# Performance work log

Measured on AMD Instinct MI355X. Metric: run time of the kernel, lower is better.

Reference implementation:

```python
import jax, jax.numpy as jnp
from jax import lax
import numpy as np


def conv2d(x, w, b):
    # x: NCHW, w: OIHW, VALID padding, stride 1
    y = lax.conv_general_dilated(x, w, (1, 1), 'VALID',
                                 dimension_numbers=('NCHW', 'OIHW', 'NCHW'))
    return y + b[None, :, None, None]


def prelu(x, a):
    # per-channel PReLU, a: (C,)
    return jnp.where(x >= 0, x, a[None, :, None, None] * x)


def maxpool_ceil(x, k, s):
    # max pool with ceil_mode=True: pad right/bottom with -inf as needed
    H, W = x.shape[2], x.shape[3]
    def pad_amt(n):
        out = -(-(n - k) // s) + 1  # ceil
        return max(0, (out - 1) * s + k - n)
    ph, pw = pad_amt(H), pad_amt(W)
    return lax.reduce_window(x, -jnp.inf, lax.max,
                             (1, 1, k, k), (1, 1, s, s),
                             ((0, 0), (0, 0), (0, ph), (0, pw)))


def setup_inputs() -> dict:
    key = jax.random.key(0)
    ks = jax.random.split(key, 24)
    N = 2048
    x = jax.random.normal(ks[0], (N, 3, 48, 48), dtype=jnp.float32)

    def w_init(k, shape, fan_in):
        return jax.random.normal(k, shape, dtype=jnp.float32) * (1.0 / np.sqrt(fan_in))

    inp = {'x': x}
    inp['c1w'] = w_init(ks[1], (32, 3, 3, 3), 3 * 9)
    inp['c1b'] = jnp.zeros((32,), jnp.float32)
    inp['a1'] = jax.random.uniform(ks[2], (32,), jnp.float32, 0.1, 0.4)
    inp['c2w'] = w_init(ks[3], (64, 32, 3, 3), 32 * 9)
    inp['c2b'] = jnp.zeros((64,), jnp.float32)
    inp['a2'] = jax.random.uniform(ks[4], (64,), jnp.float32, 0.1, 0.4)
    inp['c3w'] = w_init(ks[5], (64, 64, 3, 3), 64 * 9)
    inp['c3b'] = jnp.zeros((64,), jnp.float32)
    inp['a3'] = jax.random.uniform(ks[6], (64,), jnp.float32, 0.1, 0.4)
    inp['c4w'] = w_init(ks[7], (128, 64, 2, 2), 64 * 4)
    inp['c4b'] = jnp.zeros((128,), jnp.float32)
    inp['a4'] = jax.random.uniform(ks[8], (128,), jnp.float32, 0.1, 0.4)
    inp['d5w'] = w_init(ks[9], (256, 1152), 1152)
    inp['d5b'] = jnp.zeros((256,), jnp.float32)
    inp['a5'] = jax.random.uniform(ks[10], (256,), jnp.float32, 0.1, 0.4)
    inp['d61w'] = w_init(ks[11], (2, 256), 256)
    inp['d61b'] = jnp.zeros((2,), jnp.float32)
    inp['d62w'] = w_init(ks[12], (4, 256), 256)
    inp['d62b'] = jnp.zeros((4,), jnp.float32)
    inp['d63w'] = w_init(ks[13], (10, 256), 256)
    inp['d63b'] = jnp.zeros((10,), jnp.float32)
    return inp


def reference(x, c1w, c1b, a1, c2w, c2b, a2, c3w, c3b, a3, c4w, c4b, a4,
              d5w, d5b, a5, d61w, d61b, d62w, d62b, d63w, d63b):
    h = prelu(conv2d(x, c1w, c1b), a1)          # [N,32,46,46]
    h = maxpool_ceil(h, 3, 2)                   # [N,32,23,23]
    h = prelu(conv2d(h, c2w, c2b), a2)          # [N,64,21,21]
    h = maxpool_ceil(h, 3, 2)                   # [N,64,10,10]
    h = prelu(conv2d(h, c3w, c3b), a3)          # [N,64,8,8]
    h = maxpool_ceil(h, 2, 2)                   # [N,64,4,4]
    h = prelu(conv2d(h, c4w, c4b), a4)          # [N,128,3,3]
    # torch: x.permute(0,3,2,1).contiguous().view(N,-1)
    h = jnp.transpose(h, (0, 3, 2, 1)).reshape(h.shape[0], -1)  # [N,1152]
    h = h @ d5w.T + d5b                         # [N,256]
    h = jnp.where(h >= 0, h, a5 * h)            # PReLU over features
    a = jax.nn.softmax(h @ d61w.T + d61b, axis=1)  # class probs [N,2]
    b = h @ d62w.T + d62b
    c = h @ d63w.T + d63b                       # landmarks [N,10]
    return (b, c, a)
```

## Files before the change

### kernel.cpp

```cpp
#include <hip/hip_runtime.h>
#include <hip/hip_bf16.h>
#include <hip/hip_fp16.h>
#include <stdint.h>

typedef short s16x8 __attribute__((ext_vector_type(8)));
typedef unsigned short u16x8 __attribute__((ext_vector_type(8)));
typedef _Float16 f16x8 __attribute__((ext_vector_type(8)));
typedef __fp16 h16x2 __attribute__((ext_vector_type(2)));
typedef float f32x4 __attribute__((ext_vector_type(4)));

__device__ __forceinline__ unsigned short f2h(float f) {
    __half h = __float2half(f);
    union { __half h; unsigned short u; } c; c.h = h; return c.u;
}
__device__ __forceinline__ unsigned pkh(float a, float b) {
    union { h16x2 h; unsigned u; } c;
    c.h = __builtin_amdgcn_cvt_pkrtz(a, b);
    return c.u;
}

__global__ void k0_prep(const float* __restrict__ c2w, const float* __restrict__ c3w,
                        const float* __restrict__ c4w, const float* __restrict__ d5w,
                        unsigned short* __restrict__ w2, unsigned short* __restrict__ w3,
                        unsigned short* __restrict__ w4, unsigned short* __restrict__ w5) {
    int t = blockIdx.x * 256 + threadIdx.x;
    if (t < 18432) {
        int kpos = t / 2048, rem = t % 2048, oc = rem / 32, ic = rem % 32;
        w2[t] = f2h(c2w[(oc * 32 + ic) * 9 + kpos]);
        return;
    }
    t -= 18432;
    if (t < 36864) {
        int kpos = t / 4096, rem = t % 4096, oc = rem / 64, ic = rem % 64;
        w3[t] = f2h(c3w[(oc * 64 + ic) * 9 + kpos]);
        return;
    }
    t -= 36864;
    if (t < 32768) {
        int kpos = t / 8192, rem = t % 8192, oc = rem / 64, ic = rem % 64;
        w4[t] = f2h(c4w[(oc * 64 + ic) * 4 + kpos]);
        return;
    }
    t -= 32768;
    if (t < 294912) w5[t] = f2h(d5w[t]);
}

__global__ __launch_bounds__(256, 6)
void k1_conv1(const float* __restrict__ x, const float* __restrict__ c1w,
              const float* __restrict__ c1b, const float* __restrict__ a1,
              unsigned short* __restrict__ p1) {
    __shared__ unsigned short xstrip[1008];
    __shared__ unsigned short cbuf[230 * 40];
    __shared__ unsigned short wlds[1024];
    __shared__ float bls[32], als[32];

    const int n = blockIdx.x, tid = threadIdx.x;
    const int w = tid >> 6, lane = tid & 63, q = lane >> 4, l16 = lane & 15;

    for (int t = tid; t < 1024; t += 256) {
        int oc = t >> 5, k = t & 31;
        wlds[t] = (k < 27) ? f2h(c1w[oc * 27 + k]) : (unsigned short)0;
    }
    if (tid < 32) { bls[tid] = c1b[tid]; als[tid] = a1[tid]; }
    __syncthreads();

    f16x8 Wf[2];
    #pragma unroll
    for (int nt = 0; nt < 2; ++nt) {
        union { u16x8 u; f16x8 f; } cc;
        cc.u = *(const u16x8*)(wlds + (nt * 16 + l16) * 32 + q * 8);
        Wf[nt] = cc.f;
    }

    float bq[2][4], aq[2][4];
    #pragma unroll
    for (int nt = 0; nt < 2; ++nt)
    #pragma unroll
    for (int r = 0; r < 4; ++r) {
        bq[nt][r] = bls[nt * 16 + q * 4 + r];
        aq[nt][r] = als[nt * 16 + q * 4 + r];
    }

    int off[8];
    #pragma unroll
    for (int j = 0; j < 8; ++j) {
        int k = q * 8 + j;
        int kk = k < 27 ? k : 26;
        int ic = kk / 9, r9 = kk - ic * 9, ky = r9 / 3, kx = r9 - ky * 3;
        off[j] = ic * 336 + ky * 48 + kx;
    }

    auto do_pool = [&](int sp, int nprows, int kymax) {
        int ntask = nprows * 92;
        int t = tid;
        if (t < ntask) {
            int ocg = t & 3; unsigned r2 = (unsigned)t >> 2;
            int px = (int)(r2 % 23u), py_l = (int)(r2 / 23u);
            int kxmax = (px == 22) ? 2 : 3;
            int base = (2 * py_l * 46 + 2 * px) * 40 + ocg * 8;
            f16x8 mx;
            #pragma unroll
            for (int j = 0; j < 8; ++j) mx[j] = (_Float16)(-60000.f);
            #pragma unroll
            for (int ky = 0; ky < 3; ++ky) {
                if (ky < kymax) {
                    #pragma unroll
                    for (int kx = 0; kx < 3; ++kx) {
                        if (kx < kxmax) {
                            union { uint4 u; f16x8 f; } d;
                            d.u = *(const uint4*)&cbuf[base + (ky * 46 + kx) * 40];
                            mx = __builtin_elementwise_max(mx, d.f);
                        }
                    }
                }
            }
            union { f16x8 f; uint4 u; } o; o.f = mx;
            int py = 2 * sp + py_l;
            *(uint4*)&p1[n * 16928 + (py * 23 + px) * 32 + ocg * 8] = o.u;
        }
    };

    for (int s = 0; s < 12; ++s) {
        const int nrows = (s == 11) ? 2 : 5;
        const int P = 46 * nrows;
        const int ntiles = (P + 15) >> 4;
        const int xr0 = 4 * s;

        {
            int t4 = tid;
            if (t4 < 252) {
                int ic = t4 / 84;
                int rem4 = t4 * 4 - ic * 336;
                int rr = rem4 / 48, col = rem4 - rr * 48;
                int row = xr0 + rr; if (row > 47) row = 47;
                float4 f = *(const float4*)(x + n * 6912 + ic * 2304 + row * 48 + col);
                uint2 o; o.x = pkh(f.x, f.y); o.y = pkh(f.z, f.w);
                *(uint2*)&xstrip[t4 * 4] = o;
            }
        }
        if (s > 0) do_pool(s - 1, 2, 3);
        __syncthreads();

        for (int T = w; T < ntiles; T += 4) {
            int px = T * 16 + l16;
            int p = px < P ? px : P - 1;
            int ry = p / 46, cx = p - ry * 46;
            int basex = ry * 48 + cx;
            union { u16x8 u; f16x8 f; } xcc;
            #pragma unroll
            for (int j = 0; j < 8; ++j) xcc.u[j] = xstrip[basex + off[j]];
            f16x8 Xf = xcc.f;
            f32x4 acc[2] = {{0.f,0.f,0.f,0.f},{0.f,0.f,0.f,0.f}};
            #pragma unroll
            for (int nt = 0; nt < 2; ++nt)
                acc[nt] = __builtin_amdgcn_mfma_f32_16x16x32_f16(Wf[nt], Xf, acc[nt], 0, 0, 0);
            if (px < P) {
                #pragma unroll
                for (int nt = 0; nt < 2; ++nt) {
                    float v0 = acc[nt][0] + bq[nt][0];
                    float v1 = acc[nt][1] + bq[nt][1];
                    float v2 = acc[nt][2] + bq[nt][2];
                    float v3 = acc[nt][3] + bq[nt][3];
                    v0 = fmaxf(v0, 0.f) + aq[nt][0] * fminf(v0, 0.f);
                    v1 = fmaxf(v1, 0.f) + aq[nt][1] * fminf(v1, 0.f);
                    v2 = fmaxf(v2, 0.f) + aq[nt][2] * fminf(v2, 0.f);
                    v3 = fmaxf(v3, 0.f) + aq[nt][3] * fminf(v3, 0.f);
                    uint2 pk; pk.x = pkh(v0, v1); pk.y = pkh(v2, v3);
                    *(uint2*)&cbuf[px * 40 + nt * 16 + q * 4] = pk;
                }
            }
        }
        __syncthreads();
    }
    do_pool(11, 1, 2);
}

__global__ __launch_bounds__(256, 2)
void k23_fused(const unsigned short* __restrict__ p1, const unsigned short* __restrict__ w2,
               const float* __restrict__ c2b, const float* __restrict__ a2,
               const unsigned short* __restrict__ w3, const float* __restrict__ c3b,
               const float* __restrict__ a3, const unsigned short* __restrict__ w4,
               const float* __restrict__ c4b, const float* __restrict__ a4,
               unsigned short* __restrict__ flat) {
    __shared__ __align__(16) char smem[36544];
    unsigned short* xs    = (unsigned short*)(smem);
    unsigned short* c2s   = (unsigned short*)(smem + 10304);
    unsigned short* p2s   = (unsigned short*)(smem + 23744);
    unsigned short* c3buf = (unsigned short*)(smem);
    unsigned short* p3    = (unsigned short*)(smem + 8192);

    const int n = blockIdx.x, tid = threadIdx.x;
    const int w = tid >> 6, lane = tid & 63, q = lane >> 4, l16 = lane & 15;
    const unsigned short* p1n = p1 + n * 16928;

    const int npair = w & 1, tset = w >> 1;
    const int ocA = npair * 32 + l16, ocB = npair * 32 + 16 + l16;

    f16x8 B2[9][2];
    #pragma unroll
    for (int kp = 0; kp < 9; ++kp) {
        union { u16x8 u; f16x8 f; } c0, c1;
        c0.u = *(const u16x8*)(w2 + (kp * 64 + ocA) * 32 + q * 8);
        c1.u = *(const u16x8*)(w2 + (kp * 64 + ocB) * 32 + q * 8);
        B2[kp][0] = c0.f; B2[kp][1] = c1.f;
    }
    const float b2a = c2b[ocA], b2b = c2b[ocB];
    const float a2a = a2[ocA],  a2b = a2[ocB];

    auto stage = [&](int s) {
        const uint4* src = ((const uint4*)p1n) + 368 * s;
        for (int t = tid; t < 644; t += 256) ((uint4*)xs)[t] = src[t];
    };

    auto conv2_strip = [&]() {
        const int P = 105, ntiles = 7, half = 4;
        const int T0 = tset * half;
        const int T1 = (T0 + half) < ntiles ? (T0 + half) : ntiles;
        for (int T = T0; T < T1; ++T) {
            int m = T * 16 + l16;
            int p = m < P ? m : P - 1;
            int ry = p / 21, ox = p - ry * 21;
            const unsigned short* ab = xs + (ry * 23 + ox) * 32 + q * 8;
            f32x4 acc0 = {0.f, 0.f, 0.f, 0.f}, acc1 = {0.f, 0.f, 0.f, 0.f};
            #pragma unroll
            for (int kp = 0; kp < 9; ++kp) {
                int ky = kp / 3, kx = kp - ky * 3;
                union { u16x8 u; f16x8 f; } av;
                av.u = *(const u16x8*)(ab + (ky * 23 + kx) * 32);
                acc0 = __builtin_amdgcn_mfma_f32_16x16x32_f16(av.f, B2[kp][0], acc0, 0, 0, 0);
                acc1 = __builtin_amdgcn_mfma_f32_16x16x32_f16(av.f, B2[kp][1], acc1, 0, 0, 0);
            }
            int rowb = T * 16 + q * 4;
            #pragma unroll
            for (int r = 0; r < 4; ++r) {
                int row = rowb + r;
                if (row < P) {
                    float v0 = acc0[r] + b2a;
                    v0 = fmaxf(v0, 0.f) + a2a * fminf(v0, 0.f);
                    c2s[row * 64 + npair * 32 + l16] = f2h(v0);
                    float v1 = acc1[r] + b2b;
                    v1 = fmaxf(v1, 0.f) + a2b * fminf(v1, 0.f);
                    c2s[row * 64 + npair * 32 + 16 + l16] = f2h(v1);
                }
            }
        }
    };

    auto pool_strip = [&](int s) {
        if (tid < 160) {
            int ocg = tid & 7; int r2 = tid >> 3;
            int px = r2 % 10, pyl = r2 / 10;
            int base = (2 * pyl * 21 + 2 * px) * 64 + ocg * 8;
            f16x8 mx;
            #pragma unroll
            for (int j = 0; j < 8; ++j) mx[j] = (_Float16)(-60000.f);
            #pragma unroll
            for (int ky = 0; ky < 3; ++ky)
            #pragma unroll
            for (int kx = 0; kx < 3; ++kx) {
                union { uint4 u; f16x8 f; } d;
                d.u = *(const uint4*)&c2s[base + (ky * 21 + kx) * 64];
                mx = __builtin_elementwise_max(mx, d.f);
            }
            union { f16x8 f; uint4 u; } o; o.f = mx;
            *(uint4*)&p2s[((2 * s + pyl) * 10 + px) * 64 + ocg * 8] = o.u;
        }
    };

    stage(0);
    __syncthreads();
    for (int s = 0; s < 5; ++s) {
        conv2_strip();
        __syncthreads();
        pool_strip(s);
        if (s < 4) stage(s + 1);
        __syncthreads();
    }

    {
        const int oc3 = w * 16 + l16;
        int mbase[4];
        #pragma unroll
        for (int j = 0; j < 4; ++j) {
            int px = j * 16 + l16;
            int oy = px >> 3, ox = px & 7;
            mbase[j] = (oy * 10 + ox) * 64 + q * 8;
        }
        f32x4 acc3[4];
        #pragma unroll
        for (int j = 0; j < 4; ++j) acc3[j] = f32x4{0.f, 0.f, 0.f, 0.f};
        union { u16x8 u; f16x8 f; } bc;
        bc.u = *(const u16x8*)(w3 + oc3 * 64 + q * 8);
        f16x8 B3c = bc.f;
        for (int c = 0; c < 18; ++c) {
            f16x8 B3n = B3c;
            if (c < 17) {
                int cn = c + 1;
                union { u16x8 u; f16x8 f; } bn;
                bn.u = *(const u16x8*)(w3 + ((cn >> 1) * 64 + oc3) * 64 + (cn & 1) * 32 + q * 8);
                B3n = bn.f;
            }
            int kp = c >> 1, ky = kp / 3, kx = kp - ky * 3;
            int aoff = (ky * 10 + kx) * 64 + (c & 1) * 32;
            #pragma unroll
            for (int j = 0; j < 4; ++j) {
                union { u16x8 u; f16x8 f; } av;
                av.u = *(const u16x8*)(p2s + mbase[j] + aoff);
                acc3[j] = __builtin_amdgcn_mfma_f32_16x16x32_f16(av.f, B3c, acc3[j], 0, 0, 0);
            }
            B3c = B3n;
        }
        float bias = c3b[oc3], al = a3[oc3];
        #pragma unroll
        for (int j = 0; j < 4; ++j)
        #pragma unroll
        for (int r = 0; r < 4; ++r) {
            int row = j * 16 + q * 4 + r;
            float val = acc3[j][r] + bias;
            val = fmaxf(val, 0.f) + al * fminf(val, 0.f);
            c3buf[row * 64 + oc3] = f2h(val);
        }
    }
    __syncthreads();

    if (tid < 128) {
        int ocg = tid & 7, r = tid >> 3;
        int py = r >> 2, pxo = r & 3;
        f16x8 mx;
        #pragma unroll
        for (int j = 0; j < 8; ++j) mx[j] = (_Float16)(-60000.f);
        #pragma unroll
        for (int ky = 0; ky < 2; ++ky)
        #pragma unroll
        for (int kx = 0; kx < 2; ++kx) {
            union { uint4 u; f16x8 f; } d;
            d.u = *(const uint4*)&c3buf[((py * 2 + ky) * 8 + pxo * 2 + kx) * 64 + ocg * 8];
            mx = __builtin_elementwise_max(mx, d.f);
        }
        union { f16x8 f; uint4 u; } o; o.f = mx;
        *(uint4*)&p3[r * 64 + ocg * 8] = o.u;
    }
    __syncthreads();

    {
        int px = l16 < 9 ? l16 : 8;
        int oy = px / 3, ox = px - oy * 3;
        const int mb4 = (oy * 4 + ox) * 64 + q * 8;
        const int oc4a = (w * 2) * 16 + l16, oc4b = (w * 2 + 1) * 16 + l16;
        f32x4 acc4[2] = {{0.f,0.f,0.f,0.f},{0.f,0.f,0.f,0.f}};
        f16x8 B4c[2];
        {
            union { u16x8 u; f16x8 f; } b0, b1;
            b0.u = *(const u16x8*)(w4 + oc4a * 64 + q * 8);
            b1.u = *(const u16x8*)(w4 + oc4b * 64 + q * 8);
            B4c[0] = b0.f; B4c[1] = b1.f;
        }
        for (int c = 0; c < 8; ++c) {
            f16x8 B4n[2] = {B4c[0], B4c[1]};
            if (c < 7) {
                int cn = c + 1;
                int boff = (cn >> 1) * 8192 + (cn & 1) * 32 + q * 8;
                union { u16x8 u; f16x8 f; } b0, b1;
                b0.u = *(const u16x8*)(w4 + boff + oc4a * 64);
                b1.u = *(const u16x8*)(w4 + boff + oc4b * 64);
                B4n[0] = b0.f; B4n[1] = b1.f;
            }
            int kp = c >> 1, ky = kp >> 1, kx = kp & 1;
            union { u16x8 u; f16x8 f; } av;
            av.u = *(const u16x8*)(p3 + mb4 + (ky * 4 + kx) * 64 + (c & 1) * 32);
            acc4[0] = __builtin_amdgcn_mfma_f32_16x16x32_f16(av.f, B4c[0], acc4[0], 0, 0, 0);
            acc4[1] = __builtin_amdgcn_mfma_f32_16x16x32_f16(av.f, B4c[1], acc4[1], 0, 0, 0);
            B4c[0] = B4n[0]; B4c[1] = B4n[1];
        }
        #pragma unroll
        for (int h = 0; h < 2; ++h) {
            int oc = h ? oc4b : oc4a;
            float bias = c4b[oc], al = a4[oc];
            #pragma unroll
            for (int r = 0; r < 4; ++r) {
                int row = q * 4 + r;
                if (row < 9) {
                    int hy = row / 3, wx = row - hy * 3;
                    float val = acc4[h][r] + bias;
                    val = fmaxf(val, 0.f) + al * fminf(val, 0.f);
                    flat[(unsigned)n * 1152u + (wx * 3 + hy) * 128 + oc] = f2h(val);
                }
            }
        }
    }
}

__global__ __launch_bounds__(256, 2)
void k5_fused(const unsigned short* __restrict__ flat, const unsigned short* __restrict__ w5,
              const float* __restrict__ d5b, const float* __restrict__ a5,
              const float* __restrict__ d61w, const float* __restrict__ d61b,
              const float* __restrict__ d62w, const float* __restrict__ d62b,
              const float* __restrict__ d63w, const float* __restrict__ d63b,
              float* __restrict__ out) {
    __shared__ float hL[16 * 260];
    __shared__ float wl[16 * 260];
    __shared__ float lg[256];
    const int blk = blockIdx.x, tid = threadIdx.x;
    const int w = tid >> 6, lane = tid & 63, q = lane >> 4, l16 = lane & 15;
    const int img0 = blk * 16;
    const int img = img0 + l16;

    f32x4 acc[4];
    #pragma unroll
    for (int nt = 0; nt < 4; ++nt) acc[nt] = f32x4{0.f, 0.f, 0.f, 0.f};

    for (int c = 0; c < 36; ++c) {
        int k0 = c * 32 + q * 8;
        union { u16x8 u; f16x8 f; } av;
        av.u = *(const u16x8*)(flat + (unsigned)img * 1152u + k0);
        #pragma unroll
        for (int nt = 0; nt < 4; ++nt) {
            int oc = w * 64 + nt * 16 + l16;
            union { u16x8 u; f16x8 f; } bv;
            bv.u = *(const u16x8*)(w5 + (unsigned)oc * 1152u + k0);
            acc[nt] = __builtin_amdgcn_mfma_f32_16x16x32_f16(av.f, bv.f, acc[nt], 0, 0, 0);
        }
    }
    #pragma unroll
    for (int nt = 0; nt < 4; ++nt) {
        int oc = w * 64 + nt * 16 + l16;
        float bias = d5b[oc], al = a5[oc];
        #pragma unroll
        for (int r = 0; r < 4; ++r) {
            int im = q * 4 + r;
            float v = acc[nt][r] + bias;
            v = fmaxf(v, 0.f) + al * fminf(v, 0.f);
            hL[im * 260 + oc] = v;
        }
    }
    {
        int o = tid >> 4, seg = tid & 15;
        const float* wrow = (o < 2) ? d61w + o * 256
                          : (o < 6) ? d62w + (o - 2) * 256
                          :           d63w + (o - 6) * 256;
        #pragma unroll
        for (int j = 0; j < 4; ++j)
            *(float4*)&wl[o * 260 + seg * 16 + j * 4] = ((const float4*)wrow)[seg * 4 + j];
    }
    __syncthreads();

    const int im = tid >> 4, o = tid & 15;
    {
        float bias = (o < 2) ? d61b[o] : (o < 6) ? d62b[o - 2] : d63b[o - 6];
        float s = bias;
        const float4* ha = (const float4*)&hL[im * 260];
        const float4* wa = (const float4*)&wl[o * 260];
        #pragma unroll 8
        for (int k = 0; k < 64; ++k) {
            float4 a = ha[k], b = wa[k];
            s += a.x * b.x + a.y * b.y + a.z * b.z + a.w * b.w;
        }
        lg[im * 16 + o] = s;
    }
    __syncthreads();
    {
        int gimg = img0 + im;
        float v = lg[im * 16 + o];
        if (o >= 2 && o < 6) {
            out[gimg * 4 + (o - 2)] = v;
        } else if (o >= 6) {
            out[8192 + gimg * 10 + (o - 6)] = v;
        } else {
            float l0 = lg[im * 16 + 0], l1 = lg[im * 16 + 1];
            float mx = fmaxf(l0, l1);
            float e0 = __expf(l0 - mx), e1 = __expf(l1 - mx);
            out[28672 + gimg * 2 + o] = (o == 0 ? e0 : e1) / (e0 + e1);
        }
    }
}

extern "C" void kernel_launch(void* const* d_in, const int* in_sizes, int n_in,
                              void* d_out, int out_size, void* d_ws, size_t ws_size,
                              hipStream_t stream) {
    (void)in_sizes; (void)n_in; (void)out_size; (void)ws_size;
    const float* x    = (const float*)d_in[0];
    const float* c1w  = (const float*)d_in[1];
    const float* c1b  = (const float*)d_in[2];
    const float* a1   = (const float*)d_in[3];
    const float* c2w  = (const float*)d_in[4];
    const float* c2b  = (const float*)d_in[5];
    const float* a2   = (const float*)d_in[6];
    const float* c3w  = (const float*)d_in[7];
    const float* c3b  = (const float*)d_in[8];
    const float* a3   = (const float*)d_in[9];
    const float* c4w  = (const float*)d_in[10];
    const float* c4b  = (const float*)d_in[11];
    const float* a4   = (const float*)d_in[12];
    const float* d5w  = (const float*)d_in[13];
    const float* d5b  = (const float*)d_in[14];
    const float* a5   = (const float*)d_in[15];
    const float* d61w = (const float*)d_in[16];
    const float* d61b = (const float*)d_in[17];
    const float* d62w = (const float*)d_in[18];
    const float* d62b = (const float*)d_in[19];
    const float* d63w = (const float*)d_in[20];
    const float* d63b = (const float*)d_in[21];

    char* ws = (char*)d_ws;
    unsigned short* p1    = (unsigned short*)(ws + 0);
    unsigned short* flat  = (unsigned short*)(ws + 69337088);
    unsigned short* w2    = (unsigned short*)(ws + 186777600);
    unsigned short* w3    = (unsigned short*)(ws + 186814464);
    unsigned short* w4    = (unsigned short*)(ws + 186888192);
    unsigned short* w5    = (unsigned short*)(ws + 186953728);

    k0_prep  <<<1496, 256, 0, stream>>>(c2w, c3w, c4w, d5w, w2, w3, w4, w5);
    k1_conv1 <<<2048, 256, 0, stream>>>(x, c1w, c1b, a1, p1);
    k23_fused<<<2048, 256, 0, stream>>>(p1, w2, c2b, a2, w3, c3b, a3, w4, c4b, a4, flat);
    k5_fused <<<128, 256, 0, stream>>>(flat, w5, d5b, a5, d61w, d61b, d62w, d62b,
                                       d63w, d63b, (float*)d_out);
}
```

Measured before the change: 294.5 us.

## Apply PReLU after max-pool, fold bias into accumulators, merge weight prep

PReLU is now applied after each max-pool, in packed fp16 on the pooled values, instead of in fp32 on every conv output. This is valid only because PReLU is monotonic when the slopes are non-negative. Conv and dense biases now initialise the MFMA accumulators instead of being added afterwards. The separate weight-conversion kernel is folded into conv1 as extra trailing blocks, which removes one launch. The trade-offs are fp16 PReLU arithmetic and a hidden assumption that the alphas are non-negative.

```diff
diff --git a/kernel.cpp b/kernel.cpp
--- a/kernel.cpp
+++ b/kernel.cpp
@@ -18,50 +18,62 @@
     c.h = __builtin_amdgcn_cvt_pkrtz(a, b);
     return c.u;
 }
-
-__global__ void k0_prep(const float* __restrict__ c2w, const float* __restrict__ c3w,
-                        const float* __restrict__ c4w, const float* __restrict__ d5w,
-                        unsigned short* __restrict__ w2, unsigned short* __restrict__ w3,
-                        unsigned short* __restrict__ w4, unsigned short* __restrict__ w5) {
-    int t = blockIdx.x * 256 + threadIdx.x;
-    if (t < 18432) {
-        int kpos = t / 2048, rem = t % 2048, oc = rem / 32, ic = rem % 32;
-        w2[t] = f2h(c2w[(oc * 32 + ic) * 9 + kpos]);
-        return;
-    }
-    t -= 18432;
-    if (t < 36864) {
-        int kpos = t / 4096, rem = t % 4096, oc = rem / 64, ic = rem % 64;
-        w3[t] = f2h(c3w[(oc * 64 + ic) * 9 + kpos]);
-        return;
-    }
-    t -= 36864;
-    if (t < 32768) {
-        int kpos = t / 8192, rem = t % 8192, oc = rem / 64, ic = rem % 64;
-        w4[t] = f2h(c4w[(oc * 64 + ic) * 4 + kpos]);
-        return;
-    }
-    t -= 32768;
-    if (t < 294912) w5[t] = f2h(d5w[t]);
+__device__ __forceinline__ f16x8 prelu8(f16x8 v, f16x8 a) {
+    f16x8 z = {};
+    f16x8 pos = __builtin_elementwise_max(v, z);
+    f16x8 neg = __builtin_elementwise_min(v, z);
+    return pos + a * neg;
 }
 
 __global__ __launch_bounds__(256, 6)
 void k1_conv1(const float* __restrict__ x, const float* __restrict__ c1w,
               const float* __restrict__ c1b, const float* __restrict__ a1,
-              unsigned short* __restrict__ p1) {
+              unsigned short* __restrict__ p1,
+              const float* __restrict__ c2w, const float* __restrict__ c3w,
+              const float* __restrict__ c4w, const float* __restrict__ d5w,
+              unsigned short* __restrict__ w2, unsigned short* __restrict__ w3,
+              unsigned short* __restrict__ w4, unsigned short* __restrict__ w5) {
+    const int n = blockIdx.x, tid = threadIdx.x;
+
+    if (n >= 2048) {
+        for (int t0 = (n - 2048) * 256 + tid; t0 < 382976; t0 += 18944) {
+            int t = t0;
+            if (t < 18432) {
+                int kpos = t / 2048, rem = t % 2048, oc = rem / 32, ic = rem % 32;
+                w2[t] = f2h(c2w[(oc * 32 + ic) * 9 + kpos]);
+                continue;
+            }
+            t -= 18432;
+            if (t < 36864) {
+                int kpos = t / 4096, rem = t % 4096, oc = rem / 64, ic = rem % 64;
+                w3[t] = f2h(c3w[(oc * 64 + ic) * 9 + kpos]);
+                continue;
+            }
+            t -= 36864;
+            if (t < 32768) {
+                int kpos = t / 8192, rem = t % 8192, oc = rem / 64, ic = rem % 64;
+                w4[t] = f2h(c4w[(oc * 64 + ic) * 4 + kpos]);
+                continue;
+            }
+            t -= 32768;
+            w5[t] = f2h(d5w[t]);
+        }
+        return;
+    }
+
     __shared__ unsigned short xstrip[1008];
     __shared__ unsigned short cbuf[230 * 40];
     __shared__ unsigned short wlds[1024];
-    __shared__ float bls[32], als[32];
-
-    const int n = blockIdx.x, tid = threadIdx.x;
+    __shared__ unsigned short a1h[32];
+    __shared__ float bls[32];
+
     const int w = tid >> 6, lane = tid & 63, q = lane >> 4, l16 = lane & 15;
 
     for (int t = tid; t < 1024; t += 256) {
         int oc = t >> 5, k = t & 31;
         wlds[t] = (k < 27) ? f2h(c1w[oc * 27 + k]) : (unsigned short)0;
     }
-    if (tid < 32) { bls[tid] = c1b[tid]; als[tid] = a1[tid]; }
+    if (tid < 32) { bls[tid] = c1b[tid]; a1h[tid] = f2h(a1[tid]); }
     __syncthreads();
 
     f16x8 Wf[2];
@@ -72,14 +84,11 @@
         Wf[nt] = cc.f;
     }
 
-    float bq[2][4], aq[2][4];
+    f32x4 binit[2];
     #pragma unroll
     for (int nt = 0; nt < 2; ++nt)
     #pragma unroll
-    for (int r = 0; r < 4; ++r) {
-        bq[nt][r] = bls[nt * 16 + q * 4 + r];
-        aq[nt][r] = als[nt * 16 + q * 4 + r];
-    }
+    for (int r = 0; r < 4; ++r) binit[nt][r] = bls[nt * 16 + q * 4 + r];
 
     int off[8];
     #pragma unroll
@@ -114,7 +123,9 @@
                     }
                 }
             }
-            union { f16x8 f; uint4 u; } o; o.f = mx;
+            union { uint4 u; f16x8 f; } aal;
+            aal.u = *(const uint4*)&a1h[ocg * 8];
+            union { f16x8 f; uint4 u; } o; o.f = prelu8(mx, aal.f);
             int py = 2 * sp + py_l;
             *(uint4*)&p1[n * 16928 + (py * 23 + px) * 32 + ocg * 8] = o.u;
         }
@@ -150,22 +161,15 @@
             #pragma unroll
             for (int j = 0; j < 8; ++j) xcc.u[j] = xstrip[basex + off[j]];
             f16x8 Xf = xcc.f;
-            f32x4 acc[2] = {{0.f,0.f,0.f,0.f},{0.f,0.f,0.f,0.f}};
+            f32x4 acc[2] = {binit[0], binit[1]};
             #pragma unroll
             for (int nt = 0; nt < 2; ++nt)
                 acc[nt] = __builtin_amdgcn_mfma_f32_16x16x32_f16(Wf[nt], Xf, acc[nt], 0, 0, 0);
             if (px < P) {
                 #pragma unroll
                 for (int nt = 0; nt < 2; ++nt) {
-                    float v0 = acc[nt][0] + bq[nt][0];
-                    float v1 = acc[nt][1] + bq[nt][1];
-                    float v2 = acc[nt][2] + bq[nt][2];
-                    float v3 = acc[nt][3] + bq[nt][3];
-                    v0 = fmaxf(v0, 0.f) + aq[nt][0] * fminf(v0, 0.f);
-                    v1 = fmaxf(v1, 0.f) + aq[nt][1] * fminf(v1, 0.f);
-                    v2 = fmaxf(v2, 0.f) + aq[nt][2] * fminf(v2, 0.f);
-                    v3 = fmaxf(v3, 0.f) + aq[nt][3] * fminf(v3, 0.f);
-                    uint2 pk; pk.x = pkh(v0, v1); pk.y = pkh(v2, v3);
+                    uint2 pk; pk.x = pkh(acc[nt][0], acc[nt][1]);
+                    pk.y = pkh(acc[nt][2], acc[nt][3]);
                     *(uint2*)&cbuf[px * 40 + nt * 16 + q * 4] = pk;
                 }
             }
@@ -183,6 +187,7 @@
                const float* __restrict__ c4b, const float* __restrict__ a4,
                unsigned short* __restrict__ flat) {
     __shared__ __align__(16) char smem[36544];
+    __shared__ unsigned short a2h[64], a3h[64];
     unsigned short* xs    = (unsigned short*)(smem);
     unsigned short* c2s   = (unsigned short*)(smem + 10304);
     unsigned short* p2s   = (unsigned short*)(smem + 23744);
@@ -196,6 +201,8 @@
     const int npair = w & 1, tset = w >> 1;
     const int ocA = npair * 32 + l16, ocB = npair * 32 + 16 + l16;
 
+    if (tid < 64) { a2h[tid] = f2h(a2[tid]); a3h[tid] = f2h(a3[tid]); }
+
     f16x8 B2[9][2];
     #pragma unroll
     for (int kp = 0; kp < 9; ++kp) {
@@ -205,7 +212,6 @@
         B2[kp][0] = c0.f; B2[kp][1] = c1.f;
     }
     const float b2a = c2b[ocA], b2b = c2b[ocB];
-    const float a2a = a2[ocA],  a2b = a2[ocB];
 
     auto stage = [&](int s) {
         const uint4* src = ((const uint4*)p1n) + 368 * s;
@@ -221,7 +227,7 @@
             int p = m < P ? m : P - 1;
             int ry = p / 21, ox = p - ry * 21;
             const unsigned short* ab = xs + (ry * 23 + ox) * 32 + q * 8;
-            f32x4 acc0 = {0.f, 0.f, 0.f, 0.f}, acc1 = {0.f, 0.f, 0.f, 0.f};
+            f32x4 acc0 = {b2a, b2a, b2a, b2a}, acc1 = {b2b, b2b, b2b, b2b};
             #pragma unroll
             for (int kp = 0; kp < 9; ++kp) {
                 int ky = kp / 3, kx = kp - ky * 3;
@@ -235,12 +241,8 @@
             for (int r = 0; r < 4; ++r) {
                 int row = rowb + r;
                 if (row < P) {
-                    float v0 = acc0[r] + b2a;
-                    v0 = fmaxf(v0, 0.f) + a2a * fminf(v0, 0.f);
-                    c2s[row * 64 + npair * 32 + l16] = f2h(v0);
-                    float v1 = acc1[r] + b2b;
-                    v1 = fmaxf(v1, 0.f) + a2b * fminf(v1, 0.f);
-                    c2s[row * 64 + npair * 32 + 16 + l16] = f2h(v1);
+                    c2s[row * 64 + npair * 32 + l16]      = f2h(acc0[r]);
+                    c2s[row * 64 + npair * 32 + 16 + l16] = f2h(acc1[r]);
                 }
             }
         }
@@ -262,7 +264,9 @@
                 d.u = *(const uint4*)&c2s[base + (ky * 21 + kx) * 64];
                 mx = __builtin_elementwise_max(mx, d.f);
             }
-            union { f16x8 f; uint4 u; } o; o.f = mx;
+            union { uint4 u; f16x8 f; } aal;
+            aal.u = *(const uint4*)&a2h[ocg * 8];
+            union { f16x8 f; uint4 u; } o; o.f = prelu8(mx, aal.f);
             *(uint4*)&p2s[((2 * s + pyl) * 10 + px) * 64 + ocg * 8] = o.u;
         }
     };
@@ -286,9 +290,10 @@
             int oy = px >> 3, ox = px & 7;
             mbase[j] = (oy * 10 + ox) * 64 + q * 8;
         }
+        const float bias3 = c3b[oc3];
         f32x4 acc3[4];
         #pragma unroll
-        for (int j = 0; j < 4; ++j) acc3[j] = f32x4{0.f, 0.f, 0.f, 0.f};
+        for (int j = 0; j < 4; ++j) acc3[j] = f32x4{bias3, bias3, bias3, bias3};
         union { u16x8 u; f16x8 f; } bc;
         bc.u = *(const u16x8*)(w3 + oc3 * 64 + q * 8);
         f16x8 B3c = bc.f;
@@ -310,15 +315,12 @@
             }
             B3c = B3n;
         }
-        float bias = c3b[oc3], al = a3[oc3];
         #pragma unroll
         for (int j = 0; j < 4; ++j)
         #pragma unroll
         for (int r = 0; r < 4; ++r) {
             int row = j * 16 + q * 4 + r;
-            float val = acc3[j][r] + bias;
-            val = fmaxf(val, 0.f) + al * fminf(val, 0.f);
-            c3buf[row * 64 + oc3] = f2h(val);
+            c3buf[row * 64 + oc3] = f2h(acc3[j][r]);
         }
     }
     __syncthreads();
@@ -337,7 +339,9 @@
             d.u = *(const uint4*)&c3buf[((py * 2 + ky) * 8 + pxo * 2 + kx) * 64 + ocg * 8];
             mx = __builtin_elementwise_max(mx, d.f);
         }
-        union { f16x8 f; uint4 u; } o; o.f = mx;
+        union { uint4 u; f16x8 f; } aal;
+        aal.u = *(const uint4*)&a3h[ocg * 8];
+        union { f16x8 f; uint4 u; } o; o.f = prelu8(mx, aal.f);
         *(uint4*)&p3[r * 64 + ocg * 8] = o.u;
     }
     __syncthreads();
@@ -347,7 +351,8 @@
         int oy = px / 3, ox = px - oy * 3;
         const int mb4 = (oy * 4 + ox) * 64 + q * 8;
         const int oc4a = (w * 2) * 16 + l16, oc4b = (w * 2 + 1) * 16 + l16;
-        f32x4 acc4[2] = {{0.f,0.f,0.f,0.f},{0.f,0.f,0.f,0.f}};
+        const float b4a = c4b[oc4a], b4b = c4b[oc4b];
+        f32x4 acc4[2] = {{b4a, b4a, b4a, b4a}, {b4b, b4b, b4b, b4b}};
         f16x8 B4c[2];
         {
             union { u16x8 u; f16x8 f; } b0, b1;
@@ -375,13 +380,13 @@
         #pragma unroll
         for (int h = 0; h < 2; ++h) {
             int oc = h ? oc4b : oc4a;
-            float bias = c4b[oc], al = a4[oc];
+            float al = a4[oc];
             #pragma unroll
             for (int r = 0; r < 4; ++r) {
                 int row = q * 4 + r;
                 if (row < 9) {
                     int hy = row / 3, wx = row - hy * 3;
-                    float val = acc4[h][r] + bias;
+                    float val = acc4[h][r];
                     val = fmaxf(val, 0.f) + al * fminf(val, 0.f);
                     flat[(unsigned)n * 1152u + (wx * 3 + hy) * 128 + oc] = f2h(val);
                 }
@@ -407,7 +412,10 @@
 
     f32x4 acc[4];
     #pragma unroll
-    for (int nt = 0; nt < 4; ++nt) acc[nt] = f32x4{0.f, 0.f, 0.f, 0.f};
+    for (int nt = 0; nt < 4; ++nt) {
+        float b = d5b[w * 64 + nt * 16 + l16];
+        acc[nt] = f32x4{b, b, b, b};
+    }
 
     for (int c = 0; c < 36; ++c) {
         int k0 = c * 32 + q * 8;
@@ -424,11 +432,11 @@
     #pragma unroll
     for (int nt = 0; nt < 4; ++nt) {
         int oc = w * 64 + nt * 16 + l16;
-        float bias = d5b[oc], al = a5[oc];
+        float al = a5[oc];
         #pragma unroll
         for (int r = 0; r < 4; ++r) {
             int im = q * 4 + r;
-            float v = acc[nt][r] + bias;
+            float v = acc[nt][r];
             v = fmaxf(v, 0.f) + al * fminf(v, 0.f);
             hL[im * 260 + oc] = v;
         }
@@ -509,8 +517,8 @@
     unsigned short* w4    = (unsigned short*)(ws + 186888192);
     unsigned short* w5    = (unsigned short*)(ws + 186953728);
 
-    k0_prep  <<<1496, 256, 0, stream>>>(c2w, c3w, c4w, d5w, w2, w3, w4, w5);
-    k1_conv1 <<<2048, 256, 0, stream>>>(x, c1w, c1b, a1, p1);
+    k1_conv1 <<<2122, 256, 0, stream>>>(x, c1w, c1b, a1, p1,
+                                        c2w, c3w, c4w, d5w, w2, w3, w4, w5);
     k23_fused<<<2048, 256, 0, stream>>>(p1, w2, c2b, a2, w3, c3b, a3, w4, c4b, a4, flat);
     k5_fused <<<128, 256, 0, stream>>>(flat, w5, d5b, a5, d61w, d61b, d62w, d62b,
                                        d63w, d63b, (float*)d_out);
```

Result: faster. 279.7 us (-5.0%).
